# Kernel optimization log

Measured on AMD Instinct MI355X. Metric: run time of the kernel, lower is better.

The kernel has to match this reference:

```python
import jax, jax.numpy as jnp
import numpy as np

HEADS = 8
DIM_HEAD = 64
DIM = 512
CTX_DIM = 512
INNER = HEADS * DIM_HEAD  # 512
EPS = 1e-5


def layernorm(x, g):
    # repo-style LayerNorm: learnable gain g only, no bias, biased variance
    mean = jnp.mean(x, axis=-1, keepdims=True)
    var = jnp.var(x, axis=-1, keepdims=True)
    return (x - mean) * jax.lax.rsqrt(var + EPS) * g


def setup_inputs() -> dict:
    key = jax.random.key(0)
    ks = jax.random.split(key, 8)
    b, n, m = 2, 4096, 4096
    x = jax.random.normal(ks[0], (b, n, DIM), dtype=jnp.float32)
    context = jax.random.normal(ks[1], (b, m, CTX_DIM), dtype=jnp.float32)
    mask = jax.random.bernoulli(ks[2], 0.9, (b, m))  # bool [b, m]
    # parameters
    g_x = jnp.ones((DIM,), dtype=jnp.float32)
    null_kv = jax.random.normal(ks[3], (2, DIM_HEAD), dtype=jnp.float32)
    Wq = jax.random.normal(ks[4], (DIM, INNER), dtype=jnp.float32) * (DIM ** -0.5)
    Wkv = jax.random.normal(ks[5], (CTX_DIM, 2 * INNER), dtype=jnp.float32) * (CTX_DIM ** -0.5)
    Wo = jax.random.normal(ks[6], (INNER, DIM), dtype=jnp.float32) * (INNER ** -0.5)
    g_out = jnp.ones((DIM,), dtype=jnp.float32)
    return {"x": x, "context": context, "mask": mask, "g_x": g_x,
            "null_kv": null_kv, "Wq": Wq, "Wkv": Wkv, "Wo": Wo, "g_out": g_out}


def reference(x, context, mask, g_x, null_kv, Wq, Wkv, Wo, g_out):
    b, n, _ = x.shape
    m = context.shape[1]
    scale = DIM_HEAD ** (-0.5)  # cosine_sim=False

    xn = layernorm(x, g_x)
    ctx = context  # norm_context=False -> Identity

    q = (xn @ Wq).reshape(b, n, HEADS, DIM_HEAD)          # b n h d
    kv = (ctx @ Wkv).reshape(b, m, 2, HEADS, DIM_HEAD)     # b m 2 h d
    k, v = kv[:, :, 0], kv[:, :, 1]                        # b m h d

    # prepend the null kv token (shared across b, h)
    nk = jnp.broadcast_to(null_kv[0], (b, 1, HEADS, DIM_HEAD))
    nv = jnp.broadcast_to(null_kv[1], (b, 1, HEADS, DIM_HEAD))
    k = jnp.concatenate([nk, k], axis=1)                   # b (m+1) h d
    v = jnp.concatenate([nv, v], axis=1)

    s = jnp.sqrt(jnp.float32(scale))
    q = q * s
    k = k * s

    sim = jnp.einsum('bihd,bjhd->bhij', q, k)              # b h n (m+1)
    max_neg = -jnp.finfo(sim.dtype).max
    full_mask = jnp.pad(mask, ((0, 0), (1, 0)), constant_values=True)  # null token visible
    sim = jnp.where(full_mask[:, None, None, :], sim, max_neg)

    attn = jax.nn.softmax(sim.astype(jnp.float32), axis=-1).astype(sim.dtype)
    out = jnp.einsum('bhij,bjhd->bihd', attn, v).reshape(b, n, INNER)
    out = out @ Wo
    return layernorm(out, g_out)
```

## Files before the change

kernel.cpp:

```cpp
#include <hip/hip_runtime.h>
#include <cfloat>

typedef unsigned short u16;
typedef unsigned int u32;
typedef __bf16 v8bf16 __attribute__((ext_vector_type(8)));
typedef float v4f32 __attribute__((ext_vector_type(4)));
typedef float v16f32 __attribute__((ext_vector_type(16)));

#define MPAD 4224
#define QKS 0.42466090f
#define GRPS 1024

__device__ __forceinline__ u16 f2bf(float f) {
  union { float f; u32 u; } v; v.f = f;
  u32 u = v.u;
  u32 r = (u + 0x7FFFu + ((u >> 16) & 1u)) >> 16;
  return (u16)r;
}

__device__ __forceinline__ u32 pkbf(float lo, float hi) {
  union { float f; u32 u; } a, c;
  a.f = lo; c.f = hi;
  return __builtin_amdgcn_perm(c.u, a.u, 0x07060302);
}

__device__ __forceinline__ float asf(u32 u) {
  union { u32 u; float f; } v; v.u = u; return v.f;
}

__device__ __forceinline__ void exppack2(v16f32& sA, v16f32& sB, float& lst,
                                         v8bf16 pf[4]) {
  float rsum = 0.f;
#pragma unroll
  for (int i = 0; i < 16; i++) { float p = __builtin_amdgcn_exp2f(sA[i]); sA[i] = p; rsum += p; }
#pragma unroll
  for (int i = 0; i < 16; i++) { float p = __builtin_amdgcn_exp2f(sB[i]); sB[i] = p; rsum += p; }
  float a2 = rsum, b2 = rsum;
  asm("v_permlane32_swap_b32 %0, %1" : "+v"(a2), "+v"(b2));
  lst += a2 + b2;
#pragma unroll
  for (int kc = 0; kc < 2; kc++) {
    v16f32& s = kc ? sB : sA;
#pragma unroll
    for (int s16 = 0; s16 < 2; s16++) {
      u32 w0 = pkbf(s[s16 * 8 + 0], s[s16 * 8 + 1]);
      u32 w1 = pkbf(s[s16 * 8 + 2], s[s16 * 8 + 3]);
      u32 w2 = pkbf(s[s16 * 8 + 4], s[s16 * 8 + 5]);
      u32 w3 = pkbf(s[s16 * 8 + 6], s[s16 * 8 + 7]);
      asm("v_permlane32_swap_b32 %0, %1" : "+v"(w0), "+v"(w2));
      asm("v_permlane32_swap_b32 %0, %1" : "+v"(w1), "+v"(w3));
      union { u32 u[4]; v8bf16 v; } pu;
      pu.u[0] = w0; pu.u[1] = w1; pu.u[2] = w2; pu.u[3] = w3;
      pf[kc * 2 + s16] = pu.v;
    }
  }
}

__global__ __launch_bounds__(256) void prep_all(
    const void* __restrict__ mask, float* __restrict__ mp,
    const float* __restrict__ Wq, const float* __restrict__ Wkv,
    const float* __restrict__ Wo, u16* __restrict__ WqT,
    u16* __restrict__ WkvT, u16* __restrict__ WoT,
    const float* __restrict__ x, const float* __restrict__ g,
    u16* __restrict__ xn, const float4* __restrict__ ctx, u16* __restrict__ cb,
    const float* __restrict__ nullkv, u16* __restrict__ KVt) {
  int bb = blockIdx.x;
  int tid = threadIdx.x;
  if (bb < 33) {
    __shared__ int sflag;
    if (tid == 0) sflag = 0;
    __syncthreads();
    const unsigned char* mb = (const unsigned char*)mask;
    int loc = 0;
#pragma unroll
    for (int k = 0; k < 32; k++) {
      int i = tid * 32 + k;
      if ((i & 3) && mb[i]) loc = 1;
    }
    if (loc) sflag = 1;
    __syncthreads();
    int isbyte = sflag;
    int i = bb * 256 + tid;
    if (i >= 2 * MPAD) return;
    int b = i / MPAD, p = i - b * MPAD;
    float v;
    if (p == 0) v = 0.f;
    else if (p <= 4096) {
      int j = b * 4096 + (p - 1);
      int on = isbyte ? (((const unsigned char*)mask)[j] != 0)
                      : (((const int*)mask)[j] != 0);
      v = on ? 0.f : -1e38f;
    } else v = -1e38f;
    mp[i] = v;
  } else if (bb < 1057) {
    __shared__ float tile[32][33];
    int t = bb - 33;
    const float* in; u16* out; int N; float scale; int base;
    if (t < 256)      { in = Wq;  out = WqT;  N = 512;  scale = QKS; base = t; }
    else if (t < 768) { in = Wkv; out = WkvT; N = 1024; scale = 1.f; base = t - 256; }
    else              { in = Wo;  out = WoT;  N = 512;  scale = 1.f; base = t - 768; }
    const int K = 512;
    int ntiles = N >> 5;
    int bx = base % ntiles, by = base / ntiles;
    int n0 = bx * 32, k0 = by * 32;
    int c = tid & 31, r8 = tid >> 5;
#pragma unroll
    for (int i = 0; i < 4; i++) {
      int r = r8 + i * 8;
      tile[r][c] = in[(size_t)(k0 + r) * N + n0 + c];
    }
    __syncthreads();
#pragma unroll
    for (int i = 0; i < 4; i++) {
      int r = r8 + i * 8;
      out[(size_t)(n0 + r) * K + k0 + c] = f2bf(tile[c][r] * scale);
    }
  } else if (bb < 7201) {
    int local = bb - 1057;
    if (local < 2048) {
      int lane = tid & 63, w = tid >> 6;
      int row = local * 4 + w;
      const float* p = x + (size_t)row * 512 + lane * 8;
      float4 f0 = *(const float4*)p;
      float4 f1 = *(const float4*)(p + 4);
      float v[8] = {f0.x, f0.y, f0.z, f0.w, f1.x, f1.y, f1.z, f1.w};
      float sum = 0.f, sq = 0.f;
#pragma unroll
      for (int i = 0; i < 8; i++) { sum += v[i]; sq += v[i] * v[i]; }
#pragma unroll
      for (int m = 1; m < 64; m <<= 1) { sum += __shfl_xor(sum, m); sq += __shfl_xor(sq, m); }
      float mean = sum * (1.f / 512.f);
      float var = sq * (1.f / 512.f) - mean * mean;
      float rstd = rsqrtf(var + 1e-5f);
      const float* gp = g + lane * 8;
      u16 o[8];
#pragma unroll
      for (int i = 0; i < 8; i++) o[i] = f2bf((v[i] - mean) * rstd * gp[i]);
      *(uint4*)&xn[(size_t)row * 512 + lane * 8] = *(uint4*)o;
    } else {
      int i = (local - 2048) * 256 + tid;
      float4 f = ctx[i];
      u16 o[4] = {f2bf(f.x), f2bf(f.y), f2bf(f.z), f2bf(f.w)};
      *(uint2*)&cb[(size_t)i * 4] = *(uint2*)o;
    }
  } else {
    int bh = bb - 7201;
    size_t tb64 = ((size_t)bh * 66 + 64) * 8192;
    uint4 z = make_uint4(0, 0, 0, 0);
    for (int i = tid; i < 2048; i += 256)
      *(uint4*)&KVt[tb64 + (size_t)i * 8] = z;
    size_t tb0 = (size_t)bh * 66 * 8192;
    if (tid < 64) {
      int d = tid;
      KVt[tb0 + (size_t)(d >> 3) * 512 + (d & 7)] = f2bf(nullkv[d] * QKS);
      KVt[tb0 + 4096 + (size_t)d * 8] = f2bf(nullkv[64 + d]);
    }
  }
}

__global__ __launch_bounds__(256) void ln_to_f32(const float* __restrict__ in,
    const float* __restrict__ g, float* __restrict__ out) {
  int lane = threadIdx.x & 63, w = threadIdx.x >> 6;
  int row = blockIdx.x * 4 + w;
  const float* p = in + (size_t)row * 512 + lane * 8;
  float4 f0 = *(const float4*)p;
  float4 f1 = *(const float4*)(p + 4);
  float v[8] = {f0.x, f0.y, f0.z, f0.w, f1.x, f1.y, f1.z, f1.w};
  float sum = 0.f, sq = 0.f;
#pragma unroll
  for (int i = 0; i < 8; i++) { sum += v[i]; sq += v[i] * v[i]; }
#pragma unroll
  for (int m = 1; m < 64; m <<= 1) { sum += __shfl_xor(sum, m); sq += __shfl_xor(sq, m); }
  float mean = sum * (1.f / 512.f);
  float var = sq * (1.f / 512.f) - mean * mean;
  float rstd = rsqrtf(var + 1e-5f);
  const float* gp = g + lane * 8;
  float o[8];
#pragma unroll
  for (int i = 0; i < 8; i++) o[i] = (v[i] - mean) * rstd * gp[i];
  float* q = out + (size_t)row * 512 + lane * 8;
  *(float4*)q = make_float4(o[0], o[1], o[2], o[3]);
  *(float4*)(q + 4) = make_float4(o[4], o[5], o[6], o[7]);
}

__device__ __forceinline__ void gemm_core(const u16* __restrict__ A,
    const u16* __restrict__ Bt, u16* __restrict__ outb, float* __restrict__ outf,
    u16* __restrict__ KVt, int Ncols, int mode, int bidx,
    u16* As , u16* Bs ) {
  int tiles_n = Ncols >> 7;
  int n0 = (bidx % tiles_n) * 128;
  int m0 = (bidx / tiles_n) * 128;
  int tid = threadIdx.x;
  int lane = tid & 63, w = tid >> 6, quad = lane >> 4, l15 = lane & 15;
  int wr = w >> 1, wc = w & 1;
  int srow = tid >> 2, scol = (tid & 3) * 8;
  v4f32 acc[4][4];
#pragma unroll
  for (int i = 0; i < 4; i++)
#pragma unroll
    for (int j = 0; j < 4; j++) acc[i][j] = (v4f32){0.f, 0.f, 0.f, 0.f};

  for (int k0 = 0; k0 < 512; k0 += 32) {
    __syncthreads();
    __builtin_amdgcn_global_load_lds((const u32*)&A[(size_t)(m0 + srow) * 512 + k0 + scol],
                                     (u32*)&As[tid * 8], 16, 0, 0);
    __builtin_amdgcn_global_load_lds((const u32*)&A[(size_t)(m0 + 64 + srow) * 512 + k0 + scol],
                                     (u32*)&As[64 * 32 + tid * 8], 16, 0, 0);
    __builtin_amdgcn_global_load_lds((const u32*)&Bt[(size_t)(n0 + srow) * 512 + k0 + scol],
                                     (u32*)&Bs[tid * 8], 16, 0, 0);
    __builtin_amdgcn_global_load_lds((const u32*)&Bt[(size_t)(n0 + 64 + srow) * 512 + k0 + scol],
                                     (u32*)&Bs[64 * 32 + tid * 8], 16, 0, 0);
    __syncthreads();
    v8bf16 af[4], bf[4];
#pragma unroll
    for (int i = 0; i < 4; i++)
      af[i] = *(const v8bf16*)&As[(wr * 64 + i * 16 + l15) * 32 + quad * 8];
#pragma unroll
    for (int j = 0; j < 4; j++)
      bf[j] = *(const v8bf16*)&Bs[(wc * 64 + j * 16 + l15) * 32 + quad * 8];
#pragma unroll
    for (int i = 0; i < 4; i++)
#pragma unroll
      for (int j = 0; j < 4; j++)
        acc[i][j] = __builtin_amdgcn_mfma_f32_16x16x32_bf16(af[i], bf[j], acc[i][j], 0, 0, 0);
  }
#pragma unroll
  for (int i = 0; i < 4; i++) {
    int rbase = m0 + wr * 64 + i * 16 + quad * 4;
#pragma unroll
    for (int j = 0; j < 4; j++) {
      int col = n0 + wc * 64 + j * 16 + l15;
#pragma unroll
      for (int r = 0; r < 4; r++) {
        float v = acc[i][j][r];
        int row = rbase + r;
        if (mode == 0) {
          outb[(size_t)row * 512 + col] = f2bf(v);
        } else if (mode == 2) {
          outf[(size_t)row * 512 + col] = v;
        } else {
          int b2 = row >> 12, mr = row & 4095;
          int kk = mr + 1, kt = kk >> 6, kl = kk & 63;
          int kvsel = col >> 9, hh = (col >> 6) & 7, d = col & 63;
          size_t tb = ((size_t)(b2 * 8 + hh) * 66 + kt) * 8192;
          if (kvsel == 0) {
            int chunk = (((d >> 4) * 2 + ((d >> 3) & 1)) * 2 + (kl >> 5)) * 32 + (kl & 31);
            KVt[tb + (size_t)chunk * 8 + (d & 7)] = f2bf(v * QKS);
          } else {
            int chunk = (((kl >> 4) * 2 + ((kl >> 3) & 1)) * 2 + (d >> 5)) * 32 + (d & 31);
            KVt[tb + 4096 + (size_t)chunk * 8 + (kl & 7)] = f2bf(v);
          }
        }
      }
    }
  }
}

__global__ __launch_bounds__(256) void gemm_qkv(const u16* __restrict__ xn,
    const u16* __restrict__ WqT, u16* __restrict__ qb,
    const u16* __restrict__ cb, const u16* __restrict__ WkvT,
    u16* __restrict__ KVt) {
  __shared__ __attribute__((aligned(16))) u16 As[128 * 32];
  __shared__ __attribute__((aligned(16))) u16 Bs[128 * 32];
  int bb = blockIdx.x;
  if (bb < 256) gemm_core(xn, WqT, qb, nullptr, nullptr, 512, 0, bb, As, Bs);
  else          gemm_core(cb, WkvT, nullptr, nullptr, KVt, 1024, 1, bb - 256, As, Bs);
}

__global__ __launch_bounds__(256) void gemm_o(const u16* __restrict__ aO,
    const u16* __restrict__ WoT, float* __restrict__ OP) {
  __shared__ __attribute__((aligned(16))) u16 As[128 * 32];
  __shared__ __attribute__((aligned(16))) u16 Bs[128 * 32];
  gemm_core(aO, WoT, nullptr, OP, nullptr, 512, 2, blockIdx.x, As, Bs);
}

__global__ __launch_bounds__(256, 2) void attn_kernel(const u16* __restrict__ q,
    const u16* __restrict__ KVt, const float* __restrict__ maskbias,
    u32* __restrict__ Opart, float* __restrict__ lbuf) {
  int obid = blockIdx.x;
  int bid = (obid & 7) * 64 + (obid >> 3);
  int qt = bid & 15, bhs = bid >> 4;
  int s_p = bhs & 1, bh = bhs >> 1;
  int b = bh >> 3, hh = bh & 7;
  int tid = threadIdx.x, lane = tid & 63, w = tid >> 6;
  int m31 = lane & 31, h = (lane >> 5) & 1;
  int grp = (bh * 16 + qt) * 4 + w;
  int q0 = qt * 256 + w * 64;

  v8bf16 qf[2][4];
#pragma unroll
  for (int qg = 0; qg < 2; qg++) {
    const u16* qp = q + (size_t)(b * 4096 + q0 + qg * 32 + m31) * 512 + hh * 64 + h * 8;
#pragma unroll
    for (int ks = 0; ks < 4; ks++) qf[qg][ks] = *(const v8bf16*)&qp[ks * 16];
  }

  v16f32 acc[2][2];
#pragma unroll
  for (int qg = 0; qg < 2; qg++)
#pragma unroll
    for (int db = 0; db < 2; db++)
#pragma unroll
      for (int i = 0; i < 16; i++) acc[qg][db][i] = 0.f;
  float l_st[2] = {0.f, 0.f};

  const u16* kvb = KVt + (size_t)bh * 66 * 8192 + (size_t)(h * 64 + m31) * 8;
  const float* mg = maskbias + b * MPAD;
  int kt0 = s_p * 33;

  for (int kt = kt0; kt < kt0 + 33; ++kt) {
    const u16* tb = kvb + (size_t)kt * 8192;
    v8bf16 kf[4][2];
#pragma unroll
    for (int ks = 0; ks < 4; ks++)
#pragma unroll
      for (int kc = 0; kc < 2; kc++)
        kf[ks][kc] = *(const v8bf16*)&tb[ks * 1024 + kc * 256];
    v16f32 bias_s[2];
#pragma unroll
    for (int kc = 0; kc < 2; kc++)
#pragma unroll
      for (int gg = 0; gg < 4; gg++) {
        float4 bv = *(const float4*)&mg[kt * 64 + kc * 32 + gg * 8 + h * 4];
        bias_s[kc][gg * 4 + 0] = bv.x;
        bias_s[kc][gg * 4 + 1] = bv.y;
        bias_s[kc][gg * 4 + 2] = bv.z;
        bias_s[kc][gg * 4 + 3] = bv.w;
      }

    v8bf16 pf[2][4];
    {
      v16f32 s0 = bias_s[0], s1 = bias_s[1];
#pragma unroll
      for (int ks = 0; ks < 4; ks++) {
        s0 = __builtin_amdgcn_mfma_f32_32x32x16_bf16(kf[ks][0], qf[0][ks], s0, 0, 0, 0);
        s1 = __builtin_amdgcn_mfma_f32_32x32x16_bf16(kf[ks][1], qf[0][ks], s1, 0, 0, 0);
      }
      exppack2(s0, s1, l_st[0], pf[0]);
    }
#pragma unroll
    for (int ks = 0; ks < 4; ks++) {
      bias_s[0] = __builtin_amdgcn_mfma_f32_32x32x16_bf16(kf[ks][0], qf[1][ks], bias_s[0], 0, 0, 0);
      bias_s[1] = __builtin_amdgcn_mfma_f32_32x32x16_bf16(kf[ks][1], qf[1][ks], bias_s[1], 0, 0, 0);
    }
    exppack2(bias_s[0], bias_s[1], l_st[1], pf[1]);

    v8bf16 vf[4][2];
#pragma unroll
    for (int jb = 0; jb < 4; jb++)
#pragma unroll
      for (int db = 0; db < 2; db++)
        vf[jb][db] = *(const v8bf16*)&tb[4096 + jb * 1024 + db * 256];

#pragma unroll
    for (int qg = 0; qg < 2; qg++)
#pragma unroll
      for (int jb = 0; jb < 4; jb++)
#pragma unroll
        for (int db = 0; db < 2; db++)
          acc[qg][db] = __builtin_amdgcn_mfma_f32_32x32x16_bf16(vf[jb][db], pf[qg][jb], acc[qg][db], 0, 0, 0);
  }

  size_t ob = (size_t)(s_p * GRPS + grp) * 2048;
#pragma unroll
  for (int qg = 0; qg < 2; qg++)
#pragma unroll
    for (int db = 0; db < 2; db++)
#pragma unroll
      for (int rp = 0; rp < 8; rp++)
        Opart[ob + qg * 1024 + (size_t)(db * 8 + rp) * 64 + lane] =
            pkbf(acc[qg][db][2 * rp], acc[qg][db][2 * rp + 1]);
  if (h == 0) {
    lbuf[(size_t)(s_p * GRPS + grp) * 64 + m31] = l_st[0];
    lbuf[(size_t)(s_p * GRPS + grp) * 64 + 32 + m31] = l_st[1];
  }
}

__global__ __launch_bounds__(256) void attn_combine(const u32* __restrict__ Opart,
    const float* __restrict__ lbuf, u16* __restrict__ attnO) {
  __shared__ __attribute__((aligned(16))) u16 tl[4][2176];
  int tid = threadIdx.x, lane = tid & 63, w4 = tid >> 6;
  int m31 = lane & 31, h = (lane >> 5) & 1;
  int gq = blockIdx.x * 4 + w4;
  int qg = gq & 1, grp = gq >> 1;
  int w = grp & 3, qt = (grp >> 2) & 15, bh = grp >> 6;
  int b = bh >> 3, hh = bh & 7;

  float l0 = lbuf[(size_t)grp * 64 + qg * 32 + m31];
  float l1 = lbuf[(size_t)(GRPS + grp) * 64 + qg * 32 + m31];
  float inv = 1.f / (l0 + l1);

#pragma unroll
  for (int db = 0; db < 2; db++)
#pragma unroll
    for (int rp = 0; rp < 8; rp++) {
      u32 a = Opart[(size_t)grp * 2048 + qg * 1024 + (db * 8 + rp) * 64 + lane];
      u32 c = Opart[(size_t)(GRPS + grp) * 2048 + qg * 1024 + (db * 8 + rp) * 64 + lane];
      float fe = (asf(a << 16) + asf(c << 16)) * inv;
      float fo = (asf(a & 0xFFFF0000u) + asf(c & 0xFFFF0000u)) * inv;
      int reg = 2 * rp;
      int d0 = (reg & 3) + 8 * (reg >> 2) + 4 * h + 32 * db;
      *(u32*)&tl[w4][m31 * 68 + d0] = pkbf(fe, fo);
    }
  __builtin_amdgcn_s_waitcnt(0);
  int q0 = qt * 256 + w * 64 + qg * 32;
#pragma unroll
  for (int t2 = 0; t2 < 4; t2++) {
    int row = t2 * 8 + (lane >> 3), ch = lane & 7;
    uint4 val = *(uint4*)&tl[w4][row * 68 + ch * 8];
    *(uint4*)&attnO[(size_t)(b * 4096 + q0 + row) * 512 + hh * 64 + ch * 8] = val;
  }
}

extern "C" void kernel_launch(void* const* d_in, const int* in_sizes, int n_in,
                              void* d_out, int out_size, void* d_ws, size_t ws_size,
                              hipStream_t stream) {
  const float* x       = (const float*)d_in[0];
  const float* context = (const float*)d_in[1];
  const void*  mask    = d_in[2];
  const float* g_x     = (const float*)d_in[3];
  const float* null_kv = (const float*)d_in[4];
  const float* Wq      = (const float*)d_in[5];
  const float* Wkv     = (const float*)d_in[6];
  const float* Wo      = (const float*)d_in[7];
  const float* g_out   = (const float*)d_in[8];

  char* w = (char*)d_ws;
  size_t off = 0;
  auto alloc = [&](size_t bytes) { size_t o = off; off = (off + bytes + 255) & ~(size_t)255; return o; };

  u16* WqT    = (u16*)(w + alloc((size_t)512 * 512 * 2));
  u16* WkvT   = (u16*)(w + alloc((size_t)1024 * 512 * 2));
  u16* WoT    = (u16*)(w + alloc((size_t)512 * 512 * 2));
  float* mp   = (float*)(w + alloc((size_t)2 * MPAD * 4));
  u16* KVt    = (u16*)(w + alloc((size_t)16 * 66 * 8192 * 2));
  u16* qb     = (u16*)(w + alloc((size_t)8192 * 512 * 2));
  u16* aO     = (u16*)(w + alloc((size_t)8192 * 512 * 2));
  size_t xn_off = alloc((size_t)8192 * 512 * 2);
  size_t cb_off = alloc((size_t)8192 * 512 * 2);
  float* lbb  = (float*)(w + alloc((size_t)2 * GRPS * 64 * 4));
  u16* xn   = (u16*)(w + xn_off);
  u16* cb   = (u16*)(w + cb_off);
  u32* Opart = (u32*)(w + xn_off);
  float* OP  = (float*)(w + xn_off);

  prep_all<<<7217, 256, 0, stream>>>(mask, mp, Wq, Wkv, Wo, WqT, WkvT, WoT,
                                     x, g_x, xn, (const float4*)context, cb,
                                     null_kv, KVt);

  gemm_qkv<<<768, 256, 0, stream>>>(xn, WqT, qb, cb, WkvT, KVt);

  attn_kernel<<<512, 256, 0, stream>>>(qb, KVt, mp, Opart, lbb);
  attn_combine<<<512, 256, 0, stream>>>(Opart, lbb, aO);

  gemm_o<<<(8192 / 128) * (512 / 128), 256, 0, stream>>>(aO, WoT, OP);
  ln_to_f32<<<2048, 256, 0, stream>>>(OP, g_out, (float*)d_out);
}
```

Measured before the change: 236.7 us.

## Fuse attention combine, output GEMM and LayerNorm into one cooperative kernel

Replaces the separate attn_combine, gemm_o and ln_to_f32 launches with a single cooperative kernel of 512 blocks. Grid-wide syncs separate the three phases. The output projection now uses 128x64 tiles so each of the 512 blocks gets one tile, and each block normalizes 16 rows at the end. The attention kernel also raises wave priority around its MFMA sections with s_setprio to favour matrix issue. This aims to cut launch overhead and tail gaps between the small kernels, at the cost of two grid barriers and a smaller GEMM tile with less reuse.

```diff
diff --git a/kernel.cpp b/kernel.cpp
--- a/kernel.cpp
+++ b/kernel.cpp
@@ -1,5 +1,8 @@
 #include <hip/hip_runtime.h>
+#include <hip/hip_cooperative_groups.h>
 #include <cfloat>
+
+namespace cg = cooperative_groups;
 
 typedef unsigned short u16;
 typedef unsigned int u32;
@@ -158,33 +161,8 @@
   }
 }
 
-__global__ __launch_bounds__(256) void ln_to_f32(const float* __restrict__ in,
-    const float* __restrict__ g, float* __restrict__ out) {
-  int lane = threadIdx.x & 63, w = threadIdx.x >> 6;
-  int row = blockIdx.x * 4 + w;
-  const float* p = in + (size_t)row * 512 + lane * 8;
-  float4 f0 = *(const float4*)p;
-  float4 f1 = *(const float4*)(p + 4);
-  float v[8] = {f0.x, f0.y, f0.z, f0.w, f1.x, f1.y, f1.z, f1.w};
-  float sum = 0.f, sq = 0.f;
-#pragma unroll
-  for (int i = 0; i < 8; i++) { sum += v[i]; sq += v[i] * v[i]; }
-#pragma unroll
-  for (int m = 1; m < 64; m <<= 1) { sum += __shfl_xor(sum, m); sq += __shfl_xor(sq, m); }
-  float mean = sum * (1.f / 512.f);
-  float var = sq * (1.f / 512.f) - mean * mean;
-  float rstd = rsqrtf(var + 1e-5f);
-  const float* gp = g + lane * 8;
-  float o[8];
-#pragma unroll
-  for (int i = 0; i < 8; i++) o[i] = (v[i] - mean) * rstd * gp[i];
-  float* q = out + (size_t)row * 512 + lane * 8;
-  *(float4*)q = make_float4(o[0], o[1], o[2], o[3]);
-  *(float4*)(q + 4) = make_float4(o[4], o[5], o[6], o[7]);
-}
-
 __device__ __forceinline__ void gemm_core(const u16* __restrict__ A,
-    const u16* __restrict__ Bt, u16* __restrict__ outb, float* __restrict__ outf,
+    const u16* __restrict__ Bt, u16* __restrict__ outb,
     u16* __restrict__ KVt, int Ncols, int mode, int bidx,
     u16* As , u16* Bs ) {
   int tiles_n = Ncols >> 7;
@@ -236,8 +214,6 @@
         int row = rbase + r;
         if (mode == 0) {
           outb[(size_t)row * 512 + col] = f2bf(v);
-        } else if (mode == 2) {
-          outf[(size_t)row * 512 + col] = v;
         } else {
           int b2 = row >> 12, mr = row & 4095;
           int kk = mr + 1, kt = kk >> 6, kl = kk & 63;
@@ -263,15 +239,8 @@
   __shared__ __attribute__((aligned(16))) u16 As[128 * 32];
   __shared__ __attribute__((aligned(16))) u16 Bs[128 * 32];
   int bb = blockIdx.x;
-  if (bb < 256) gemm_core(xn, WqT, qb, nullptr, nullptr, 512, 0, bb, As, Bs);
-  else          gemm_core(cb, WkvT, nullptr, nullptr, KVt, 1024, 1, bb - 256, As, Bs);
-}
-
-__global__ __launch_bounds__(256) void gemm_o(const u16* __restrict__ aO,
-    const u16* __restrict__ WoT, float* __restrict__ OP) {
-  __shared__ __attribute__((aligned(16))) u16 As[128 * 32];
-  __shared__ __attribute__((aligned(16))) u16 Bs[128 * 32];
-  gemm_core(aO, WoT, nullptr, OP, nullptr, 512, 2, blockIdx.x, As, Bs);
+  if (bb < 256) gemm_core(xn, WqT, qb, nullptr, 512, 0, bb, As, Bs);
+  else          gemm_core(cb, WkvT, nullptr, KVt, 1024, 1, bb - 256, As, Bs);
 }
 
 __global__ __launch_bounds__(256, 2) void attn_kernel(const u16* __restrict__ q,
@@ -331,18 +300,22 @@
     v8bf16 pf[2][4];
     {
       v16f32 s0 = bias_s[0], s1 = bias_s[1];
+      __builtin_amdgcn_s_setprio(1);
 #pragma unroll
       for (int ks = 0; ks < 4; ks++) {
         s0 = __builtin_amdgcn_mfma_f32_32x32x16_bf16(kf[ks][0], qf[0][ks], s0, 0, 0, 0);
         s1 = __builtin_amdgcn_mfma_f32_32x32x16_bf16(kf[ks][1], qf[0][ks], s1, 0, 0, 0);
       }
+      __builtin_amdgcn_s_setprio(0);
       exppack2(s0, s1, l_st[0], pf[0]);
     }
+    __builtin_amdgcn_s_setprio(1);
 #pragma unroll
     for (int ks = 0; ks < 4; ks++) {
       bias_s[0] = __builtin_amdgcn_mfma_f32_32x32x16_bf16(kf[ks][0], qf[1][ks], bias_s[0], 0, 0, 0);
       bias_s[1] = __builtin_amdgcn_mfma_f32_32x32x16_bf16(kf[ks][1], qf[1][ks], bias_s[1], 0, 0, 0);
     }
+    __builtin_amdgcn_s_setprio(0);
     exppack2(bias_s[0], bias_s[1], l_st[1], pf[1]);
 
     v8bf16 vf[4][2];
@@ -352,6 +325,7 @@
       for (int db = 0; db < 2; db++)
         vf[jb][db] = *(const v8bf16*)&tb[4096 + jb * 1024 + db * 256];
 
+    __builtin_amdgcn_s_setprio(1);
 #pragma unroll
     for (int qg = 0; qg < 2; qg++)
 #pragma unroll
@@ -359,6 +333,7 @@
 #pragma unroll
         for (int db = 0; db < 2; db++)
           acc[qg][db] = __builtin_amdgcn_mfma_f32_32x32x16_bf16(vf[jb][db], pf[qg][jb], acc[qg][db], 0, 0, 0);
+    __builtin_amdgcn_s_setprio(0);
   }
 
   size_t ob = (size_t)(s_p * GRPS + grp) * 2048;
@@ -376,39 +351,127 @@
   }
 }
 
-__global__ __launch_bounds__(256) void attn_combine(const u32* __restrict__ Opart,
-    const float* __restrict__ lbuf, u16* __restrict__ attnO) {
-  __shared__ __attribute__((aligned(16))) u16 tl[4][2176];
-  int tid = threadIdx.x, lane = tid & 63, w4 = tid >> 6;
-  int m31 = lane & 31, h = (lane >> 5) & 1;
-  int gq = blockIdx.x * 4 + w4;
-  int qg = gq & 1, grp = gq >> 1;
-  int w = grp & 3, qt = (grp >> 2) & 15, bh = grp >> 6;
-  int b = bh >> 3, hh = bh & 7;
-
-  float l0 = lbuf[(size_t)grp * 64 + qg * 32 + m31];
-  float l1 = lbuf[(size_t)(GRPS + grp) * 64 + qg * 32 + m31];
-  float inv = 1.f / (l0 + l1);
-
-#pragma unroll
-  for (int db = 0; db < 2; db++)
-#pragma unroll
-    for (int rp = 0; rp < 8; rp++) {
-      u32 a = Opart[(size_t)grp * 2048 + qg * 1024 + (db * 8 + rp) * 64 + lane];
-      u32 c = Opart[(size_t)(GRPS + grp) * 2048 + qg * 1024 + (db * 8 + rp) * 64 + lane];
-      float fe = (asf(a << 16) + asf(c << 16)) * inv;
-      float fo = (asf(a & 0xFFFF0000u) + asf(c & 0xFFFF0000u)) * inv;
-      int reg = 2 * rp;
-      int d0 = (reg & 3) + 8 * (reg >> 2) + 4 * h + 32 * db;
-      *(u32*)&tl[w4][m31 * 68 + d0] = pkbf(fe, fo);
-    }
-  __builtin_amdgcn_s_waitcnt(0);
-  int q0 = qt * 256 + w * 64 + qg * 32;
-#pragma unroll
-  for (int t2 = 0; t2 < 4; t2++) {
-    int row = t2 * 8 + (lane >> 3), ch = lane & 7;
-    uint4 val = *(uint4*)&tl[w4][row * 68 + ch * 8];
-    *(uint4*)&attnO[(size_t)(b * 4096 + q0 + row) * 512 + hh * 64 + ch * 8] = val;
+__global__ __launch_bounds__(256) void tail_fused(const u32* __restrict__ Opart,
+    const float* __restrict__ lbuf, u16* __restrict__ attnO,
+    const u16* __restrict__ WoT, float* __restrict__ OP,
+    const float* __restrict__ g, float* __restrict__ out) {
+  __shared__ __attribute__((aligned(16))) unsigned char smem[17408];
+  cg::grid_group grid = cg::this_grid();
+  int tid = threadIdx.x;
+
+  {
+    u16 (*tl)[2176] = (u16(*)[2176])smem;
+    int lane = tid & 63, w4 = tid >> 6;
+    int m31 = lane & 31, h = (lane >> 5) & 1;
+    int gq = blockIdx.x * 4 + w4;
+    int qg = gq & 1, grp = gq >> 1;
+    int w = grp & 3, qt = (grp >> 2) & 15, bh = grp >> 6;
+    int b = bh >> 3, hh = bh & 7;
+
+    float l0 = lbuf[(size_t)grp * 64 + qg * 32 + m31];
+    float l1 = lbuf[(size_t)(GRPS + grp) * 64 + qg * 32 + m31];
+    float inv = 1.f / (l0 + l1);
+
+#pragma unroll
+    for (int db = 0; db < 2; db++)
+#pragma unroll
+      for (int rp = 0; rp < 8; rp++) {
+        u32 a = Opart[(size_t)grp * 2048 + qg * 1024 + (db * 8 + rp) * 64 + lane];
+        u32 c = Opart[(size_t)(GRPS + grp) * 2048 + qg * 1024 + (db * 8 + rp) * 64 + lane];
+        float fe = (asf(a << 16) + asf(c << 16)) * inv;
+        float fo = (asf(a & 0xFFFF0000u) + asf(c & 0xFFFF0000u)) * inv;
+        int reg = 2 * rp;
+        int d0 = (reg & 3) + 8 * (reg >> 2) + 4 * h + 32 * db;
+        *(u32*)&tl[w4][m31 * 68 + d0] = pkbf(fe, fo);
+      }
+    __builtin_amdgcn_s_waitcnt(0);
+    int q0 = qt * 256 + w * 64 + qg * 32;
+#pragma unroll
+    for (int t2 = 0; t2 < 4; t2++) {
+      int row = t2 * 8 + (lane >> 3), ch = lane & 7;
+      uint4 val = *(uint4*)&tl[w4][row * 68 + ch * 8];
+      *(uint4*)&attnO[(size_t)(b * 4096 + q0 + row) * 512 + hh * 64 + ch * 8] = val;
+    }
+  }
+  __threadfence();
+  grid.sync();
+
+  {
+    u16* As = (u16*)smem;
+    u16* Bs = (u16*)(smem + 8192);
+    int bidx = blockIdx.x;
+    int n0 = (bidx & 7) * 64;
+    int m0 = (bidx >> 3) * 128;
+    int lane = tid & 63, w = tid >> 6, quad = lane >> 4, l15 = lane & 15;
+    int srow = tid >> 2, scol = (tid & 3) * 8;
+    v4f32 acc[2][4];
+#pragma unroll
+    for (int i = 0; i < 2; i++)
+#pragma unroll
+      for (int j = 0; j < 4; j++) acc[i][j] = (v4f32){0.f, 0.f, 0.f, 0.f};
+
+    for (int k0 = 0; k0 < 512; k0 += 32) {
+      __syncthreads();
+      __builtin_amdgcn_global_load_lds((const u32*)&attnO[(size_t)(m0 + srow) * 512 + k0 + scol],
+                                       (u32*)&As[tid * 8], 16, 0, 0);
+      __builtin_amdgcn_global_load_lds((const u32*)&attnO[(size_t)(m0 + 64 + srow) * 512 + k0 + scol],
+                                       (u32*)&As[64 * 32 + tid * 8], 16, 0, 0);
+      __builtin_amdgcn_global_load_lds((const u32*)&WoT[(size_t)(n0 + srow) * 512 + k0 + scol],
+                                       (u32*)&Bs[tid * 8], 16, 0, 0);
+      __syncthreads();
+      v8bf16 af[2], bf[4];
+#pragma unroll
+      for (int i = 0; i < 2; i++)
+        af[i] = *(const v8bf16*)&As[(w * 32 + i * 16 + l15) * 32 + quad * 8];
+#pragma unroll
+      for (int j = 0; j < 4; j++)
+        bf[j] = *(const v8bf16*)&Bs[(j * 16 + l15) * 32 + quad * 8];
+#pragma unroll
+      for (int i = 0; i < 2; i++)
+#pragma unroll
+        for (int j = 0; j < 4; j++)
+          acc[i][j] = __builtin_amdgcn_mfma_f32_16x16x32_bf16(af[i], bf[j], acc[i][j], 0, 0, 0);
+    }
+#pragma unroll
+    for (int i = 0; i < 2; i++) {
+      int rbase = m0 + w * 32 + i * 16 + quad * 4;
+#pragma unroll
+      for (int j = 0; j < 4; j++) {
+        int col = n0 + j * 16 + l15;
+#pragma unroll
+        for (int r = 0; r < 4; r++)
+          OP[(size_t)(rbase + r) * 512 + col] = acc[i][j][r];
+      }
+    }
+  }
+  __threadfence();
+  grid.sync();
+
+  {
+    int lane = tid & 63, w = tid >> 6;
+#pragma unroll
+    for (int it = 0; it < 4; it++) {
+      int row = blockIdx.x * 16 + it * 4 + w;
+      const float* p = OP + (size_t)row * 512 + lane * 8;
+      float4 f0 = *(const float4*)p;
+      float4 f1 = *(const float4*)(p + 4);
+      float v[8] = {f0.x, f0.y, f0.z, f0.w, f1.x, f1.y, f1.z, f1.w};
+      float sum = 0.f, sq = 0.f;
+#pragma unroll
+      for (int i = 0; i < 8; i++) { sum += v[i]; sq += v[i] * v[i]; }
+#pragma unroll
+      for (int m = 1; m < 64; m <<= 1) { sum += __shfl_xor(sum, m); sq += __shfl_xor(sq, m); }
+      float mean = sum * (1.f / 512.f);
+      float var = sq * (1.f / 512.f) - mean * mean;
+      float rstd = rsqrtf(var + 1e-5f);
+      const float* gp = g + lane * 8;
+      float o[8];
+#pragma unroll
+      for (int i = 0; i < 8; i++) o[i] = (v[i] - mean) * rstd * gp[i];
+      float* qp = out + (size_t)row * 512 + lane * 8;
+      *(float4*)qp = make_float4(o[0], o[1], o[2], o[3]);
+      *(float4*)(qp + 4) = make_float4(o[4], o[5], o[6], o[7]);
+    }
   }
 }
 
@@ -451,8 +514,10 @@
   gemm_qkv<<<768, 256, 0, stream>>>(xn, WqT, qb, cb, WkvT, KVt);
 
   attn_kernel<<<512, 256, 0, stream>>>(qb, KVt, mp, Opart, lbb);
-  attn_combine<<<512, 256, 0, stream>>>(Opart, lbb, aO);
-
-  gemm_o<<<(8192 / 128) * (512 / 128), 256, 0, stream>>>(aO, WoT, OP);
-  ln_to_f32<<<2048, 256, 0, stream>>>(OP, g_out, (float*)d_out);
-}
+
+  float* outp = (float*)d_out;
+  void* args[] = {(void*)&Opart, (void*)&lbb, (void*)&aO, (void*)&WoT,
+                  (void*)&OP, (void*)&g_out, (void*)&outp};
+  hipLaunchCooperativeKernel((const void*)tail_fused, dim3(512), dim3(256),
+                             args, 0, stream);
+}
```

After: 481.8 us. 104% more time.
